# Performance work log

Measured on AMD Instinct MI355X. Metric: run time of the kernel, lower is better.

The kernel has to match this reference:

```python
import jax, jax.numpy as jnp
from jax import lax
import numpy as np

WIN = 11
PAD = WIN // 2
SIGMA = 1.5
GAMMA = 50.0


def _gauss_1d():
    x = jnp.arange(WIN, dtype=jnp.float32) - PAD
    g = jnp.exp(-(x * x) / (2.0 * SIGMA * SIGMA))
    return g / jnp.sum(g)


def _dwconv_gauss(x):
    # depthwise separable 11x11 gaussian blur, zero ('SAME') padding, NCHW
    C = x.shape[1]
    g = _gauss_1d()
    kh = jnp.tile(g.reshape(1, 1, WIN, 1), (C, 1, 1, 1))
    kw = jnp.tile(g.reshape(1, 1, 1, WIN), (C, 1, 1, 1))
    dn = ('NCHW', 'OIHW', 'NCHW')
    x = lax.conv_general_dilated(x, kh, (1, 1), [(PAD, PAD), (0, 0)],
                                 dimension_numbers=dn, feature_group_count=C)
    x = lax.conv_general_dilated(x, kw, (1, 1), [(0, 0), (PAD, PAD)],
                                 dimension_numbers=dn, feature_group_count=C)
    return x


def ssim(img1, img2):
    C1, C2 = 0.01 ** 2, 0.03 ** 2
    mu1 = _dwconv_gauss(img1)
    mu2 = _dwconv_gauss(img2)
    mu1_sq, mu2_sq, mu12 = mu1 * mu1, mu2 * mu2, mu1 * mu2
    sigma1_sq = _dwconv_gauss(img1 * img1) - mu1_sq
    sigma2_sq = _dwconv_gauss(img2 * img2) - mu2_sq
    sigma12 = _dwconv_gauss(img1 * img2) - mu12
    ssim_map = ((2 * mu12 + C1) * (2 * sigma12 + C2)) / (
        (mu1_sq + mu2_sq + C1) * (sigma1_sq + sigma2_sq + C2))
    return jnp.mean(ssim_map)


def warp(img, disp, x_dist, y_dist):
    # bilinear sample img at (x + x_dist*disp, y + y_dist*disp), border clamp
    B, C, H, W = img.shape
    d = disp[:, 0]  # [B,H,W]
    xs = jnp.arange(W, dtype=img.dtype)[None, None, :]
    ys = jnp.arange(H, dtype=img.dtype)[None, :, None]
    xn = jnp.clip(xs + x_dist * d, 0.0, W - 1.0)
    yn = jnp.clip(ys + y_dist * d, 0.0, H - 1.0)
    x0 = jnp.floor(xn)
    y0 = jnp.floor(yn)
    wx = xn - x0
    wy = yn - y0
    x0i = x0.astype(jnp.int32)
    y0i = y0.astype(jnp.int32)
    x1i = jnp.minimum(x0i + 1, W - 1)
    y1i = jnp.minimum(y0i + 1, H - 1)
    imh = jnp.transpose(img, (0, 2, 3, 1))  # [B,H,W,C]
    b = jnp.arange(B)[:, None, None]
    v00 = imh[b, y0i, x0i]
    v01 = imh[b, y0i, x1i]
    v10 = imh[b, y1i, x0i]
    v11 = imh[b, y1i, x1i]
    wx = wx[..., None]
    wy = wy[..., None]
    out = (v00 * (1 - wx) * (1 - wy) + v01 * wx * (1 - wy)
           + v10 * (1 - wx) * wy + v11 * wx * wy)
    return jnp.transpose(out, (0, 3, 1, 2))


def smooth_loss(disp, img, gamma):
    ddx = jnp.abs(disp[:, :, :, :-1] - disp[:, :, :, 1:])
    ddy = jnp.abs(disp[:, :, :-1, :] - disp[:, :, 1:, :])
    idx = jnp.mean(jnp.abs(img[:, :, :, :-1] - img[:, :, :, 1:]), axis=1, keepdims=True)
    idy = jnp.mean(jnp.abs(img[:, :, :-1, :] - img[:, :, 1:, :]), axis=1, keepdims=True)
    return jnp.mean(ddx * jnp.exp(-gamma * idx)) + jnp.mean(ddy * jnp.exp(-gamma * idy))


def l1(a, b):
    return jnp.mean(jnp.abs(a - b))


def setup_inputs() -> dict:
    key = jax.random.key(0)
    ks = jax.random.split(key, 8)
    B, H, W = 8, 512, 1024
    MAXD = 64.0
    return {
        'disp_l': jax.random.uniform(ks[0], (B, 1, H, W), jnp.float32) * MAXD,
        'disp_r': jax.random.uniform(ks[1], (B, 1, H, W), jnp.float32) * MAXD,
        'disp_ld2': jax.random.uniform(ks[2], (B, 1, H // 2, W // 2), jnp.float32) * (MAXD / 2),
        'disp_rd2': jax.random.uniform(ks[3], (B, 1, H // 2, W // 2), jnp.float32) * (MAXD / 2),
        'img_l': jax.random.uniform(ks[4], (B, 3, H, W), jnp.float32),
        'img_r': jax.random.uniform(ks[5], (B, 3, H, W), jnp.float32),
        'img_ld2': jax.random.uniform(ks[6], (B, 3, H // 2, W // 2), jnp.float32),
        'img_rd2': jax.random.uniform(ks[7], (B, 3, H // 2, W // 2), jnp.float32),
    }


def reference(disp_l, disp_r, disp_ld2, disp_rd2, img_l, img_r, img_ld2, img_rd2):
    img_ld2_warp = warp(img_rd2, disp_ld2, x_dist=-1.0, y_dist=0.0)
    img_rd2_warp = warp(img_ld2, disp_rd2, x_dist=1.0, y_dist=0.0)
    pm_d2 = l1(img_ld2_warp, img_ld2) + l1(img_rd2_warp, img_rd2)
    smooth_d2 = smooth_loss(disp_ld2, img_ld2, GAMMA) + smooth_loss(disp_rd2, img_rd2, GAMMA)

    img_l_warp = warp(img_r, disp_l, x_dist=-1.0, y_dist=0.0)
    img_r_warp = warp(img_l, disp_r, x_dist=1.0, y_dist=0.0)
    pm = l1(img_l_warp, img_l) + l1(img_r_warp, img_r)
    smooth = smooth_loss(disp_l, img_l, GAMMA) + smooth_loss(disp_r, img_r, GAMMA)
    ssim_loss = 1.0 - (ssim(img_l_warp, img_l) + ssim(img_r_warp, img_r)) / 2.0

    full_loss = pm_d2 + 0.1 * smooth_d2 + pm + ssim_loss + 0.1 * smooth
    monitor_loss = 5.0 * pm + ssim_loss
    return (full_loss, monitor_loss)
```

## Files before the change

kernel.cpp:

```cpp
#include <hip/hip_runtime.h>

#define B_ 8
#define C_ 3
#define H_ 512
#define W_ 1024
#define H2_ 256
#define W2_ 512
#define GAMMA_ 50.0f
#define NSUB 4

typedef __attribute__((ext_vector_type(2))) float v2f;


template <int NV>
__device__ __forceinline__ void reduce_acc(float (&v)[NV], double* acc, const int (&qidx)[NV]) {
    __shared__ float sred[NV][4];
    const int lane = threadIdx.x & 63;
    const int wave = threadIdx.x >> 6;
#pragma unroll
    for (int o = 32; o > 0; o >>= 1)
#pragma unroll
        for (int q = 0; q < NV; q++) v[q] += __shfl_down(v[q], o, 64);
    if (lane == 0)
#pragma unroll
        for (int q = 0; q < NV; q++) sred[q][wave] = v[q];
    __syncthreads();
    if (threadIdx.x == 0) {
        const int sub = blockIdx.x & (NSUB - 1);
#pragma unroll
        for (int q = 0; q < NV; q++) {
            float s = sred[q][0] + sred[q][1] + sred[q][2] + sred[q][3];
            atomicAdd(&acc[qidx[q] * NSUB + sub], (double)s);
        }
    }
}

__global__ void init_acc(double* acc) {
    if (threadIdx.x < 7 * NSUB) acc[threadIdx.x] = 0.0;
}

#define G0 0.0010283804f
#define G1 0.0075987582f
#define G2 0.0360007882f
#define G3 0.1093606949f
#define G4 0.2130055428f
#define G5 0.2660117248f

#define NHALF (B_ * H2_ * (W2_ / 4))
#define NSMOOTH (B_ * H_ * (W_ / 4))
#define NTOT (NHALF + NSMOOTH)

__global__ __launch_bounds__(256) void small_losses_kernel(
    const float* __restrict__ dL2, const float* __restrict__ dR2,
    const float* __restrict__ iL2, const float* __restrict__ iR2,
    const float* __restrict__ dL, const float* __restrict__ dR,
    const float* __restrict__ iL, const float* __restrict__ iR, double* acc) {
    float pm = 0.f, sx2 = 0.f, sy2 = 0.f, sxf = 0.f, syf = 0.f;
    for (int i = blockIdx.x * blockDim.x + threadIdx.x; i < NTOT;
         i += gridDim.x * blockDim.x) {
        if (i < NHALF) {
            const int W4 = W2_ >> 2;
            const int HW = H2_ * W2_;
            const int xq = i % W4;
            const int x4 = xq << 2;
            const int yz = i / W4;
            const int y = yz % H2_;
            const int b = yz / H2_;
            const int p0 = (b * H2_ + y) * W2_ + x4;
            const int ib = ((b * C_) * H2_ + y) * W2_ + x4;
            const bool lastx = (x4 + 4 == W2_);
            const bool lasty = (y == H2_ - 1);

            float dl[5], dr[5];
            *(float4*)dl = *(const float4*)(dL2 + p0);
            *(float4*)dr = *(const float4*)(dR2 + p0);
            dl[4] = lastx ? 0.f : dL2[p0 + 4];
            dr[4] = lastx ? 0.f : dR2[p0 + 4];

            int xl0[4], xl1[4], xr0[4], xr1[4];
            float wxl[4], wxr[4];
#pragma unroll
            for (int t = 0; t < 4; t++) {
                float xn = fminf(fmaxf((float)(x4 + t) - dl[t], 0.f), (float)(W2_ - 1));
                float xf = floorf(xn);
                wxl[t] = xn - xf;
                xl0[t] = (int)xf;
                xl1[t] = xl0[t] + (xl0[t] < W2_ - 1 ? 1 : 0);
                float xm = fminf(fmaxf((float)(x4 + t) + dr[t], 0.f), (float)(W2_ - 1));
                float xg = floorf(xm);
                wxr[t] = xm - xg;
                xr0[t] = (int)xg;
                xr1[t] = xr0[t] + (xr0[t] < W2_ - 1 ? 1 : 0);
            }

            float axL[4] = {0, 0, 0, 0}, axR[4] = {0, 0, 0, 0};
            float ayL[4] = {0, 0, 0, 0}, ayR[4] = {0, 0, 0, 0};
#pragma unroll
            for (int ch = 0; ch < C_; ch++) {
                const float* pL = iL2 + ib + ch * HW;
                const float* pR = iR2 + ib + ch * HW;
                float vL[5], vR[5];
                *(float4*)vL = *(const float4*)pL;
                *(float4*)vR = *(const float4*)pR;
                vL[4] = lastx ? 0.f : pL[4];
                vR[4] = lastx ? 0.f : pR[4];
#pragma unroll
                for (int t = 0; t < 4; t++) {
                    axL[t] += fabsf(vL[t] - vL[t + 1]);
                    axR[t] += fabsf(vR[t] - vR[t + 1]);
                }
                if (!lasty) {
                    float wLr[4], wRr[4];
                    *(float4*)wLr = *(const float4*)(pL + W2_);
                    *(float4*)wRr = *(const float4*)(pR + W2_);
#pragma unroll
                    for (int t = 0; t < 4; t++) {
                        ayL[t] += fabsf(vL[t] - wLr[t]);
                        ayR[t] += fabsf(vR[t] - wRr[t]);
                    }
                }
                const float* gLrow = iR2 + ib - x4 + ch * HW;
                const float* gRrow = iL2 + ib - x4 + ch * HW;
#pragma unroll
                for (int t = 0; t < 4; t++) {
                    float wv = gLrow[xl0[t]] * (1.f - wxl[t]) + gLrow[xl1[t]] * wxl[t];
                    pm += fabsf(wv - vL[t]);
                    float wv2 = gRrow[xr0[t]] * (1.f - wxr[t]) + gRrow[xr1[t]] * wxr[t];
                    pm += fabsf(wv2 - vR[t]);
                }
            }
            const int nx = lastx ? 3 : 4;
#pragma unroll
            for (int t = 0; t < 4; t++) {
                if (t < nx) {
                    sx2 += fabsf(dl[t] - dl[t + 1]) * __expf(-GAMMA_ * (axL[t] * (1.f / 3.f)));
                    sx2 += fabsf(dr[t] - dr[t + 1]) * __expf(-GAMMA_ * (axR[t] * (1.f / 3.f)));
                }
            }
            if (!lasty) {
                float el[4], er[4];
                *(float4*)el = *(const float4*)(dL2 + p0 + W2_);
                *(float4*)er = *(const float4*)(dR2 + p0 + W2_);
#pragma unroll
                for (int t = 0; t < 4; t++) {
                    sy2 += fabsf(dl[t] - el[t]) * __expf(-GAMMA_ * (ayL[t] * (1.f / 3.f)));
                    sy2 += fabsf(dr[t] - er[t]) * __expf(-GAMMA_ * (ayR[t] * (1.f / 3.f)));
                }
            }
        } else {
            const int s = i - NHALF;
            const int W4 = W_ >> 2;
            const int HW = H_ * W_;
            const int xq = s % W4;
            const int x4 = xq << 2;
            const int yz = s / W4;
            const int y = yz % H_;
            const int b = yz / H_;
            const int p0 = (b * H_ + y) * W_ + x4;
            const int ib = ((b * C_) * H_ + y) * W_ + x4;
            const bool lastx = (x4 + 4 == W_);
            const bool lasty = (y == H_ - 1);

            float axL[4] = {0, 0, 0, 0}, axR[4] = {0, 0, 0, 0};
            float ayL[4] = {0, 0, 0, 0}, ayR[4] = {0, 0, 0, 0};
#pragma unroll
            for (int ch = 0; ch < C_; ch++) {
                const float* pL = iL + ib + ch * HW;
                const float* pR = iR + ib + ch * HW;
                float vL[5], vR[5];
                *(float4*)vL = *(const float4*)pL;
                *(float4*)vR = *(const float4*)pR;
                vL[4] = lastx ? 0.f : pL[4];
                vR[4] = lastx ? 0.f : pR[4];
#pragma unroll
                for (int t = 0; t < 4; t++) {
                    axL[t] += fabsf(vL[t] - vL[t + 1]);
                    axR[t] += fabsf(vR[t] - vR[t + 1]);
                }
                if (!lasty) {
                    float wLr[4], wRr[4];
                    *(float4*)wLr = *(const float4*)(pL + W_);
                    *(float4*)wRr = *(const float4*)(pR + W_);
#pragma unroll
                    for (int t = 0; t < 4; t++) {
                        ayL[t] += fabsf(vL[t] - wLr[t]);
                        ayR[t] += fabsf(vR[t] - wRr[t]);
                    }
                }
            }
            float dl[5], dr[5];
            *(float4*)dl = *(const float4*)(dL + p0);
            *(float4*)dr = *(const float4*)(dR + p0);
            dl[4] = lastx ? 0.f : dL[p0 + 4];
            dr[4] = lastx ? 0.f : dR[p0 + 4];
            const int nx = lastx ? 3 : 4;
#pragma unroll
            for (int t = 0; t < 4; t++) {
                if (t < nx) {
                    sxf += fabsf(dl[t] - dl[t + 1]) * __expf(-GAMMA_ * (axL[t] * (1.f / 3.f)));
                    sxf += fabsf(dr[t] - dr[t + 1]) * __expf(-GAMMA_ * (axR[t] * (1.f / 3.f)));
                }
            }
            if (!lasty) {
                float el[4], er[4];
                *(float4*)el = *(const float4*)(dL + p0 + W_);
                *(float4*)er = *(const float4*)(dR + p0 + W_);
#pragma unroll
                for (int t = 0; t < 4; t++) {
                    syf += fabsf(dl[t] - el[t]) * __expf(-GAMMA_ * (ayL[t] * (1.f / 3.f)));
                    syf += fabsf(dr[t] - er[t]) * __expf(-GAMMA_ * (ayR[t] * (1.f / 3.f)));
                }
            }
        }
    }
    float vals[5] = {pm, sx2, sy2, sxf, syf};
    const int qidx[5] = {0, 1, 2, 4, 5};
    reduce_acc<5>(vals, acc, qidx);
}

#define TH 16
#define TW 64
#define HALO_H (TH + 10)
#define HALO_W (TW + 10)
#define HALO_N (HALO_H * HALO_W)
#define VW 75

__device__ __forceinline__ int swz(int ridx) {
    return ridx ^ (((ridx >> 3) & 1) << 1) ^ ((ridx >> 4) & 1);
}

__global__ __launch_bounds__(256) void ssim_pm_kernel(const float* __restrict__ img_l,
                                                      const float* __restrict__ img_r,
                                                      const float* __restrict__ disp_l,
                                                      const float* __restrict__ disp_r,
                                                      double* acc) {
    __shared__ float2 sAB[HALO_N];
    __shared__ float4 vF[TH * VW];

    const int z = blockIdx.z;
    const int b = z >> 1;
    const int pair = z & 1;
    const float* samp = (pair == 0) ? img_r : img_l;
    const float* targ = (pair == 0) ? img_l : img_r;
    const float* disp = (pair == 0) ? disp_l : disp_r;
    const float sign = (pair == 0) ? -1.f : 1.f;

    const int x0t = blockIdx.x * TW;
    const int y0t = blockIdx.y * TH;

    const float gg[11] = {G0, G1, G2, G3, G4, G5, G4, G3, G2, G1, G0};
    v2f w01[14], w23[14];
#pragma unroll
    for (int k = 0; k < 14; ++k) {
        w01[k].x = (k <= 10) ? gg[k] : 0.f;
        w01[k].y = (k >= 1 && k <= 11) ? gg[k - 1] : 0.f;
        w23[k].x = (k >= 2 && k <= 12) ? gg[k - 2] : 0.f;
        w23[k].y = (k >= 3) ? gg[k - 3] : 0.f;
    }

    int riy[8], gxa[8], gxb[8];
    float wxs[8];
    {
        const int bHW = b * (H_ * W_);
#pragma unroll
        for (int it = 0; it < 8; ++it) {
            const int idx = threadIdx.x + 256 * it;
            riy[it] = -1;
            if (idx < HALO_N) {
                const int i = idx / HALO_W;
                const int j = idx - i * HALO_W;
                const int iy = y0t + i - 5;
                const int ix = x0t + j - 5;
                if (iy >= 0 && iy < H_ && ix >= 0 && ix < W_) {
                    const int r = iy * W_ + ix;
                    riy[it] = r;
                    const float d = disp[bHW + r];
                    float xn = fminf(fmaxf((float)ix + sign * d, 0.f), (float)(W_ - 1));
                    float xf = floorf(xn);
                    wxs[it] = xn - xf;
                    const int xi = (int)xf;
                    gxa[it] = iy * W_ + xi;
                    gxb[it] = gxa[it] + (xi < W_ - 1 ? 1 : 0);
                }
            }
        }
    }

    float pa0[8], pa1[8], pbv[8];
    auto prefetch = [&](int c) {
        const int cb = (b * C_ + c) * (H_ * W_);
#pragma unroll
        for (int it = 0; it < 8; ++it) {
            const int idx = threadIdx.x + 256 * it;
            if (idx < HALO_N && riy[it] >= 0) {
                pbv[it] = targ[cb + riy[it]];
                pa0[it] = samp[cb + gxa[it]];
                pa1[it] = samp[cb + gxb[it]];
            }
        }
    };

    float ssim_loc = 0.f, pm_loc = 0.f;

    const int hr = threadIdx.x >> 4;
    const int hc0 = (threadIdx.x & 15) << 2;

    prefetch(0);

#pragma unroll 1
    for (int c = 0; c < C_; ++c) {
#pragma unroll
        for (int it = 0; it < 8; ++it) {
            const int idx = threadIdx.x + 256 * it;
            if (idx < HALO_N) {
                float av = 0.f, bv = 0.f;
                if (riy[it] >= 0) {
                    const float wx = wxs[it];
                    av = pa0[it] * (1.f - wx) + pa1[it] * wx;
                    bv = pbv[it];
                }
                sAB[idx] = make_float2(av, bv);
            }
        }
        __syncthreads();

        if (c + 1 < C_) prefetch(c + 1);

#pragma unroll
        for (int it = 0; it < 2; ++it) {
            const int t = threadIdx.x + 256 * it;
            if (t < 4 * HALO_W) {
                const int q = t / HALO_W;
                const int j = t - q * HALO_W;
                const int r0 = q * 4;
                const bool jc = (j >= 5 && j < 69);
                v2f amA = 0.f, bmA = 0.f, ssA = 0.f, abA = 0.f;
                v2f amB = 0.f, bmB = 0.f, ssB = 0.f, abB = 0.f;
#pragma unroll
                for (int k = 0; k < 14; ++k) {
                    const float2 p = sAB[(r0 + k) * HALO_W + j];
                    const float sq = fmaf(p.y, p.y, p.x * p.x);
                    const float ab = p.x * p.y;
                    const v2f wA = w01[k], wB = w23[k];
                    amA += wA * p.x;
                    bmA += wA * p.y;
                    ssA += wA * sq;
                    abA += wA * ab;
                    amB += wB * p.x;
                    bmB += wB * p.y;
                    ssB += wB * sq;
                    abB += wB * ab;
                    if (k >= 5 && k <= 8) {
                        if (jc) pm_loc += fabsf(p.x - p.y);
                    }
                }
                const int rb = r0 * VW + j;
                vF[swz(rb)] = make_float4(amA.x, bmA.x, ssA.x, abA.x);
                vF[swz(rb + VW)] = make_float4(amA.y, bmA.y, ssA.y, abA.y);
                vF[swz(rb + 2 * VW)] = make_float4(amB.x, bmB.x, ssB.x, abB.x);
                vF[swz(rb + 3 * VW)] = make_float4(amB.y, bmB.y, ssB.y, abB.y);
            }
        }
        __syncthreads();

        {
            const int rowb = hr * VW + hc0;
            v2f m1A = 0.f, m2A = 0.f, qsA = 0.f, q12A = 0.f;
            v2f m1B = 0.f, m2B = 0.f, qsB = 0.f, q12B = 0.f;
#pragma unroll
            for (int k = 0; k < 14; ++k) {
                const float4 f = vF[swz(rowb + k)];
                const v2f wA = w01[k], wB = w23[k];
                m1A += wA * f.x;
                m2A += wA * f.y;
                qsA += wA * f.z;
                q12A += wA * f.w;
                m1B += wB * f.x;
                m2B += wB * f.y;
                qsB += wB * f.z;
                q12B += wB * f.w;
            }
            const float C1 = 1e-4f, C2 = 9e-4f;
            {
                const v2f mu1sq = m1A * m1A, mu2sq = m2A * m2A, mu12 = m1A * m2A;
                const v2f s12 = q12A - mu12, ss = qsA - mu1sq - mu2sq;
                const v2f num = (2.f * mu12 + C1) * (2.f * s12 + C2);
                const v2f den = (mu1sq + mu2sq + C1) * (ss + C2);
                const v2f r = num / den;
                ssim_loc += r.x + r.y;
            }
            {
                const v2f mu1sq = m1B * m1B, mu2sq = m2B * m2B, mu12 = m1B * m2B;
                const v2f s12 = q12B - mu12, ss = qsB - mu1sq - mu2sq;
                const v2f num = (2.f * mu12 + C1) * (2.f * s12 + C2);
                const v2f den = (mu1sq + mu2sq + C1) * (ss + C2);
                const v2f r = num / den;
                ssim_loc += r.x + r.y;
            }
        }
    }

    float vals[2] = {ssim_loc, pm_loc};
    const int qidx[2] = {6, 3};
    reduce_acc<2>(vals, acc, qidx);
}

__global__ void finalize_kernel(const double* __restrict__ acc, float* __restrict__ out) {
    if (threadIdx.x == 0 && blockIdx.x == 0) {
        double q[7];
        for (int i = 0; i < 7; i++) {
            q[i] = 0.0;
            for (int s = 0; s < NSUB; s++) q[i] += acc[i * NSUB + s];
        }
        const double N2 = (double)B_ * C_ * H2_ * W2_;
        const double Nx2 = (double)B_ * H2_ * (W2_ - 1);
        const double Ny2 = (double)B_ * (H2_ - 1) * W2_;
        const double N1 = (double)B_ * C_ * H_ * W_;
        const double Nx1 = (double)B_ * H_ * (W_ - 1);
        const double Ny1 = (double)B_ * (H_ - 1) * W_;
        double pm_d2 = q[0] / N2;
        double smooth_d2 = q[1] / Nx2 + q[2] / Ny2;
        double pm = q[3] / N1;
        double smooth = q[4] / Nx1 + q[5] / Ny1;
        double ssim_loss = 1.0 - q[6] / (2.0 * N1);
        double full = pm_d2 + 0.1 * smooth_d2 + pm + ssim_loss + 0.1 * smooth;
        double mon = 5.0 * pm + ssim_loss;
        out[0] = (float)full;
        out[1] = (float)mon;
    }
}

extern "C" void kernel_launch(void* const* d_in, const int* in_sizes, int n_in,
                              void* d_out, int out_size, void* d_ws, size_t ws_size,
                              hipStream_t stream) {
    const float* disp_l = (const float*)d_in[0];
    const float* disp_r = (const float*)d_in[1];
    const float* disp_ld2 = (const float*)d_in[2];
    const float* disp_rd2 = (const float*)d_in[3];
    const float* img_l = (const float*)d_in[4];
    const float* img_r = (const float*)d_in[5];
    const float* img_ld2 = (const float*)d_in[6];
    const float* img_rd2 = (const float*)d_in[7];
    double* acc = (double*)d_ws;
    float* out = (float*)d_out;

    hipLaunchKernelGGL(init_acc, dim3(1), dim3(64), 0, stream, acc);

    hipLaunchKernelGGL(small_losses_kernel, dim3(2048), dim3(256), 0, stream,
                       disp_ld2, disp_rd2, img_ld2, img_rd2,
                       disp_l, disp_r, img_l, img_r, acc);

    dim3 grid(W_ / TW, H_ / TH, 2 * B_);
    hipLaunchKernelGGL(ssim_pm_kernel, grid, dim3(256), 0, stream,
                       img_l, img_r, disp_l, disp_r, acc);

    hipLaunchKernelGGL(finalize_kernel, dim3(1), dim3(1), 0, stream, acc, out);
}
```

Baseline: 231.1 us.

## Fuse small-loss and SSIM kernels into one interleaved-grid launch

```diff
diff --git a/kernel.cpp b/kernel.cpp
--- a/kernel.cpp
+++ b/kernel.cpp
@@ -46,178 +46,6 @@
 #define G4 0.2130055428f
 #define G5 0.2660117248f
 
-#define NHALF (B_ * H2_ * (W2_ / 4))
-#define NSMOOTH (B_ * H_ * (W_ / 4))
-#define NTOT (NHALF + NSMOOTH)
-
-__global__ __launch_bounds__(256) void small_losses_kernel(
-    const float* __restrict__ dL2, const float* __restrict__ dR2,
-    const float* __restrict__ iL2, const float* __restrict__ iR2,
-    const float* __restrict__ dL, const float* __restrict__ dR,
-    const float* __restrict__ iL, const float* __restrict__ iR, double* acc) {
-    float pm = 0.f, sx2 = 0.f, sy2 = 0.f, sxf = 0.f, syf = 0.f;
-    for (int i = blockIdx.x * blockDim.x + threadIdx.x; i < NTOT;
-         i += gridDim.x * blockDim.x) {
-        if (i < NHALF) {
-            const int W4 = W2_ >> 2;
-            const int HW = H2_ * W2_;
-            const int xq = i % W4;
-            const int x4 = xq << 2;
-            const int yz = i / W4;
-            const int y = yz % H2_;
-            const int b = yz / H2_;
-            const int p0 = (b * H2_ + y) * W2_ + x4;
-            const int ib = ((b * C_) * H2_ + y) * W2_ + x4;
-            const bool lastx = (x4 + 4 == W2_);
-            const bool lasty = (y == H2_ - 1);
-
-            float dl[5], dr[5];
-            *(float4*)dl = *(const float4*)(dL2 + p0);
-            *(float4*)dr = *(const float4*)(dR2 + p0);
-            dl[4] = lastx ? 0.f : dL2[p0 + 4];
-            dr[4] = lastx ? 0.f : dR2[p0 + 4];
-
-            int xl0[4], xl1[4], xr0[4], xr1[4];
-            float wxl[4], wxr[4];
-#pragma unroll
-            for (int t = 0; t < 4; t++) {
-                float xn = fminf(fmaxf((float)(x4 + t) - dl[t], 0.f), (float)(W2_ - 1));
-                float xf = floorf(xn);
-                wxl[t] = xn - xf;
-                xl0[t] = (int)xf;
-                xl1[t] = xl0[t] + (xl0[t] < W2_ - 1 ? 1 : 0);
-                float xm = fminf(fmaxf((float)(x4 + t) + dr[t], 0.f), (float)(W2_ - 1));
-                float xg = floorf(xm);
-                wxr[t] = xm - xg;
-                xr0[t] = (int)xg;
-                xr1[t] = xr0[t] + (xr0[t] < W2_ - 1 ? 1 : 0);
-            }
-
-            float axL[4] = {0, 0, 0, 0}, axR[4] = {0, 0, 0, 0};
-            float ayL[4] = {0, 0, 0, 0}, ayR[4] = {0, 0, 0, 0};
-#pragma unroll
-            for (int ch = 0; ch < C_; ch++) {
-                const float* pL = iL2 + ib + ch * HW;
-                const float* pR = iR2 + ib + ch * HW;
-                float vL[5], vR[5];
-                *(float4*)vL = *(const float4*)pL;
-                *(float4*)vR = *(const float4*)pR;
-                vL[4] = lastx ? 0.f : pL[4];
-                vR[4] = lastx ? 0.f : pR[4];
-#pragma unroll
-                for (int t = 0; t < 4; t++) {
-                    axL[t] += fabsf(vL[t] - vL[t + 1]);
-                    axR[t] += fabsf(vR[t] - vR[t + 1]);
-                }
-                if (!lasty) {
-                    float wLr[4], wRr[4];
-                    *(float4*)wLr = *(const float4*)(pL + W2_);
-                    *(float4*)wRr = *(const float4*)(pR + W2_);
-#pragma unroll
-                    for (int t = 0; t < 4; t++) {
-                        ayL[t] += fabsf(vL[t] - wLr[t]);
-                        ayR[t] += fabsf(vR[t] - wRr[t]);
-                    }
-                }
-                const float* gLrow = iR2 + ib - x4 + ch * HW;
-                const float* gRrow = iL2 + ib - x4 + ch * HW;
-#pragma unroll
-                for (int t = 0; t < 4; t++) {
-                    float wv = gLrow[xl0[t]] * (1.f - wxl[t]) + gLrow[xl1[t]] * wxl[t];
-                    pm += fabsf(wv - vL[t]);
-                    float wv2 = gRrow[xr0[t]] * (1.f - wxr[t]) + gRrow[xr1[t]] * wxr[t];
-                    pm += fabsf(wv2 - vR[t]);
-                }
-            }
-            const int nx = lastx ? 3 : 4;
-#pragma unroll
-            for (int t = 0; t < 4; t++) {
-                if (t < nx) {
-                    sx2 += fabsf(dl[t] - dl[t + 1]) * __expf(-GAMMA_ * (axL[t] * (1.f / 3.f)));
-                    sx2 += fabsf(dr[t] - dr[t + 1]) * __expf(-GAMMA_ * (axR[t] * (1.f / 3.f)));
-                }
-            }
-            if (!lasty) {
-                float el[4], er[4];
-                *(float4*)el = *(const float4*)(dL2 + p0 + W2_);
-                *(float4*)er = *(const float4*)(dR2 + p0 + W2_);
-#pragma unroll
-                for (int t = 0; t < 4; t++) {
-                    sy2 += fabsf(dl[t] - el[t]) * __expf(-GAMMA_ * (ayL[t] * (1.f / 3.f)));
-                    sy2 += fabsf(dr[t] - er[t]) * __expf(-GAMMA_ * (ayR[t] * (1.f / 3.f)));
-                }
-            }
-        } else {
-            const int s = i - NHALF;
-            const int W4 = W_ >> 2;
-            const int HW = H_ * W_;
-            const int xq = s % W4;
-            const int x4 = xq << 2;
-            const int yz = s / W4;
-            const int y = yz % H_;
-            const int b = yz / H_;
-            const int p0 = (b * H_ + y) * W_ + x4;
-            const int ib = ((b * C_) * H_ + y) * W_ + x4;
-            const bool lastx = (x4 + 4 == W_);
-            const bool lasty = (y == H_ - 1);
-
-            float axL[4] = {0, 0, 0, 0}, axR[4] = {0, 0, 0, 0};
-            float ayL[4] = {0, 0, 0, 0}, ayR[4] = {0, 0, 0, 0};
-#pragma unroll
-            for (int ch = 0; ch < C_; ch++) {
-                const float* pL = iL + ib + ch * HW;
-                const float* pR = iR + ib + ch * HW;
-                float vL[5], vR[5];
-                *(float4*)vL = *(const float4*)pL;
-                *(float4*)vR = *(const float4*)pR;
-                vL[4] = lastx ? 0.f : pL[4];
-                vR[4] = lastx ? 0.f : pR[4];
-#pragma unroll
-                for (int t = 0; t < 4; t++) {
-                    axL[t] += fabsf(vL[t] - vL[t + 1]);
-                    axR[t] += fabsf(vR[t] - vR[t + 1]);
-                }
-                if (!lasty) {
-                    float wLr[4], wRr[4];
-                    *(float4*)wLr = *(const float4*)(pL + W_);
-                    *(float4*)wRr = *(const float4*)(pR + W_);
-#pragma unroll
-                    for (int t = 0; t < 4; t++) {
-                        ayL[t] += fabsf(vL[t] - wLr[t]);
-                        ayR[t] += fabsf(vR[t] - wRr[t]);
-                    }
-                }
-            }
-            float dl[5], dr[5];
-            *(float4*)dl = *(const float4*)(dL + p0);
-            *(float4*)dr = *(const float4*)(dR + p0);
-            dl[4] = lastx ? 0.f : dL[p0 + 4];
-            dr[4] = lastx ? 0.f : dR[p0 + 4];
-            const int nx = lastx ? 3 : 4;
-#pragma unroll
-            for (int t = 0; t < 4; t++) {
-                if (t < nx) {
-                    sxf += fabsf(dl[t] - dl[t + 1]) * __expf(-GAMMA_ * (axL[t] * (1.f / 3.f)));
-                    sxf += fabsf(dr[t] - dr[t + 1]) * __expf(-GAMMA_ * (axR[t] * (1.f / 3.f)));
-                }
-            }
-            if (!lasty) {
-                float el[4], er[4];
-                *(float4*)el = *(const float4*)(dL + p0 + W_);
-                *(float4*)er = *(const float4*)(dR + p0 + W_);
-#pragma unroll
-                for (int t = 0; t < 4; t++) {
-                    syf += fabsf(dl[t] - el[t]) * __expf(-GAMMA_ * (ayL[t] * (1.f / 3.f)));
-                    syf += fabsf(dr[t] - er[t]) * __expf(-GAMMA_ * (ayR[t] * (1.f / 3.f)));
-                }
-            }
-        }
-    }
-    float vals[5] = {pm, sx2, sy2, sxf, syf};
-    const int qidx[5] = {0, 1, 2, 4, 5};
-    reduce_acc<5>(vals, acc, qidx);
-}
-
 #define TH 16
 #define TW 64
 #define HALO_H (TH + 10)
@@ -225,19 +53,197 @@
 #define HALO_N (HALO_H * HALO_W)
 #define VW 75
 
+#define NHALF (B_ * H2_ * (W2_ / 4))
+#define NSMOOTH (B_ * H_ * (W_ / 4))
+#define NTOT (NHALF + NSMOOTH)
+#define NSMALLBLK 1024
+#define NSSIMBLK 8192
+
 __device__ __forceinline__ int swz(int ridx) {
     return ridx ^ (((ridx >> 3) & 1) << 1) ^ ((ridx >> 4) & 1);
 }
 
-__global__ __launch_bounds__(256) void ssim_pm_kernel(const float* __restrict__ img_l,
-                                                      const float* __restrict__ img_r,
-                                                      const float* __restrict__ disp_l,
-                                                      const float* __restrict__ disp_r,
-                                                      double* acc) {
+__global__ __launch_bounds__(256) void fused_kernel(
+    const float* __restrict__ disp_l, const float* __restrict__ disp_r,
+    const float* __restrict__ dL2, const float* __restrict__ dR2,
+    const float* __restrict__ img_l, const float* __restrict__ img_r,
+    const float* __restrict__ iL2, const float* __restrict__ iR2, double* acc) {
     __shared__ float2 sAB[HALO_N];
     __shared__ float4 vF[TH * VW];
 
-    const int z = blockIdx.z;
+    const int bid = blockIdx.x;
+    const int grp = bid / 9;
+    const int rem = bid - grp * 9;
+
+    if (rem == 8) {
+        float pm = 0.f, sx2 = 0.f, sy2 = 0.f, sxf = 0.f, syf = 0.f;
+        for (int i = grp * blockDim.x + threadIdx.x; i < NTOT;
+             i += NSMALLBLK * blockDim.x) {
+            if (i < NHALF) {
+                const int W4 = W2_ >> 2;
+                const int HW = H2_ * W2_;
+                const int xq = i % W4;
+                const int x4 = xq << 2;
+                const int yz = i / W4;
+                const int y = yz % H2_;
+                const int b = yz / H2_;
+                const int p0 = (b * H2_ + y) * W2_ + x4;
+                const int ib = ((b * C_) * H2_ + y) * W2_ + x4;
+                const bool lastx = (x4 + 4 == W2_);
+                const bool lasty = (y == H2_ - 1);
+
+                float dl[5], dr[5];
+                *(float4*)dl = *(const float4*)(dL2 + p0);
+                *(float4*)dr = *(const float4*)(dR2 + p0);
+                dl[4] = lastx ? 0.f : dL2[p0 + 4];
+                dr[4] = lastx ? 0.f : dR2[p0 + 4];
+
+                int xl0[4], xl1[4], xr0[4], xr1[4];
+                float wxl[4], wxr[4];
+#pragma unroll
+                for (int t = 0; t < 4; t++) {
+                    float xn = fminf(fmaxf((float)(x4 + t) - dl[t], 0.f), (float)(W2_ - 1));
+                    float xf = floorf(xn);
+                    wxl[t] = xn - xf;
+                    xl0[t] = (int)xf;
+                    xl1[t] = xl0[t] + (xl0[t] < W2_ - 1 ? 1 : 0);
+                    float xm = fminf(fmaxf((float)(x4 + t) + dr[t], 0.f), (float)(W2_ - 1));
+                    float xg = floorf(xm);
+                    wxr[t] = xm - xg;
+                    xr0[t] = (int)xg;
+                    xr1[t] = xr0[t] + (xr0[t] < W2_ - 1 ? 1 : 0);
+                }
+
+                float axL[4] = {0, 0, 0, 0}, axR[4] = {0, 0, 0, 0};
+                float ayL[4] = {0, 0, 0, 0}, ayR[4] = {0, 0, 0, 0};
+#pragma unroll
+                for (int ch = 0; ch < C_; ch++) {
+                    const float* pL = iL2 + ib + ch * HW;
+                    const float* pR = iR2 + ib + ch * HW;
+                    float vL[5], vR[5];
+                    *(float4*)vL = *(const float4*)pL;
+                    *(float4*)vR = *(const float4*)pR;
+                    vL[4] = lastx ? 0.f : pL[4];
+                    vR[4] = lastx ? 0.f : pR[4];
+#pragma unroll
+                    for (int t = 0; t < 4; t++) {
+                        axL[t] += fabsf(vL[t] - vL[t + 1]);
+                        axR[t] += fabsf(vR[t] - vR[t + 1]);
+                    }
+                    if (!lasty) {
+                        float wLr[4], wRr[4];
+                        *(float4*)wLr = *(const float4*)(pL + W2_);
+                        *(float4*)wRr = *(const float4*)(pR + W2_);
+#pragma unroll
+                        for (int t = 0; t < 4; t++) {
+                            ayL[t] += fabsf(vL[t] - wLr[t]);
+                            ayR[t] += fabsf(vR[t] - wRr[t]);
+                        }
+                    }
+                    const float* gLrow = iR2 + ib - x4 + ch * HW;
+                    const float* gRrow = iL2 + ib - x4 + ch * HW;
+#pragma unroll
+                    for (int t = 0; t < 4; t++) {
+                        float wv = gLrow[xl0[t]] * (1.f - wxl[t]) + gLrow[xl1[t]] * wxl[t];
+                        pm += fabsf(wv - vL[t]);
+                        float wv2 = gRrow[xr0[t]] * (1.f - wxr[t]) + gRrow[xr1[t]] * wxr[t];
+                        pm += fabsf(wv2 - vR[t]);
+                    }
+                }
+                const int nx = lastx ? 3 : 4;
+#pragma unroll
+                for (int t = 0; t < 4; t++) {
+                    if (t < nx) {
+                        sx2 += fabsf(dl[t] - dl[t + 1]) * __expf(-GAMMA_ * (axL[t] * (1.f / 3.f)));
+                        sx2 += fabsf(dr[t] - dr[t + 1]) * __expf(-GAMMA_ * (axR[t] * (1.f / 3.f)));
+                    }
+                }
+                if (!lasty) {
+                    float el[4], er[4];
+                    *(float4*)el = *(const float4*)(dL2 + p0 + W2_);
+                    *(float4*)er = *(const float4*)(dR2 + p0 + W2_);
+#pragma unroll
+                    for (int t = 0; t < 4; t++) {
+                        sy2 += fabsf(dl[t] - el[t]) * __expf(-GAMMA_ * (ayL[t] * (1.f / 3.f)));
+                        sy2 += fabsf(dr[t] - er[t]) * __expf(-GAMMA_ * (ayR[t] * (1.f / 3.f)));
+                    }
+                }
+            } else {
+                const int s = i - NHALF;
+                const int W4 = W_ >> 2;
+                const int HW = H_ * W_;
+                const int xq = s % W4;
+                const int x4 = xq << 2;
+                const int yz = s / W4;
+                const int y = yz % H_;
+                const int b = yz / H_;
+                const int p0 = (b * H_ + y) * W_ + x4;
+                const int ib = ((b * C_) * H_ + y) * W_ + x4;
+                const bool lastx = (x4 + 4 == W_);
+                const bool lasty = (y == H_ - 1);
+
+                float axL[4] = {0, 0, 0, 0}, axR[4] = {0, 0, 0, 0};
+                float ayL[4] = {0, 0, 0, 0}, ayR[4] = {0, 0, 0, 0};
+#pragma unroll
+                for (int ch = 0; ch < C_; ch++) {
+                    const float* pL = img_l + ib + ch * HW;
+                    const float* pR = img_r + ib + ch * HW;
+                    float vL[5], vR[5];
+                    *(float4*)vL = *(const float4*)pL;
+                    *(float4*)vR = *(const float4*)pR;
+                    vL[4] = lastx ? 0.f : pL[4];
+                    vR[4] = lastx ? 0.f : pR[4];
+#pragma unroll
+                    for (int t = 0; t < 4; t++) {
+                        axL[t] += fabsf(vL[t] - vL[t + 1]);
+                        axR[t] += fabsf(vR[t] - vR[t + 1]);
+                    }
+                    if (!lasty) {
+                        float wLr[4], wRr[4];
+                        *(float4*)wLr = *(const float4*)(pL + W_);
+                        *(float4*)wRr = *(const float4*)(pR + W_);
+#pragma unroll
+                        for (int t = 0; t < 4; t++) {
+                            ayL[t] += fabsf(vL[t] - wLr[t]);
+                            ayR[t] += fabsf(vR[t] - wRr[t]);
+                        }
+                    }
+                }
+                float dl[5], dr[5];
+                *(float4*)dl = *(const float4*)(disp_l + p0);
+                *(float4*)dr = *(const float4*)(disp_r + p0);
+                dl[4] = lastx ? 0.f : disp_l[p0 + 4];
+                dr[4] = lastx ? 0.f : disp_r[p0 + 4];
+                const int nx = lastx ? 3 : 4;
+#pragma unroll
+                for (int t = 0; t < 4; t++) {
+                    if (t < nx) {
+                        sxf += fabsf(dl[t] - dl[t + 1]) * __expf(-GAMMA_ * (axL[t] * (1.f / 3.f)));
+                        sxf += fabsf(dr[t] - dr[t + 1]) * __expf(-GAMMA_ * (axR[t] * (1.f / 3.f)));
+                    }
+                }
+                if (!lasty) {
+                    float el[4], er[4];
+                    *(float4*)el = *(const float4*)(disp_l + p0 + W_);
+                    *(float4*)er = *(const float4*)(disp_r + p0 + W_);
+#pragma unroll
+                    for (int t = 0; t < 4; t++) {
+                        syf += fabsf(dl[t] - el[t]) * __expf(-GAMMA_ * (ayL[t] * (1.f / 3.f)));
+                        syf += fabsf(dr[t] - er[t]) * __expf(-GAMMA_ * (ayR[t] * (1.f / 3.f)));
+                    }
+                }
+            }
+        }
+        float vals[5] = {pm, sx2, sy2, sxf, syf};
+        const int qidx[5] = {0, 1, 2, 4, 5};
+        reduce_acc<5>(vals, acc, qidx);
+        return;
+    }
+
+    const int sid = grp * 8 + rem;
+    const int bx = sid & 15;
+    const int by = (sid >> 4) & 31;
+    const int z = sid >> 9;
     const int b = z >> 1;
     const int pair = z & 1;
     const float* samp = (pair == 0) ? img_r : img_l;
@@ -245,8 +251,8 @@
     const float* disp = (pair == 0) ? disp_l : disp_r;
     const float sign = (pair == 0) ? -1.f : 1.f;
 
-    const int x0t = blockIdx.x * TW;
-    const int y0t = blockIdx.y * TH;
+    const int x0t = bx * TW;
+    const int y0t = by * TH;
 
     const float gg[11] = {G0, G1, G2, G3, G4, G5, G4, G3, G2, G1, G0};
     v2f w01[14], w23[14];
@@ -446,13 +452,9 @@
 
     hipLaunchKernelGGL(init_acc, dim3(1), dim3(64), 0, stream, acc);
 
-    hipLaunchKernelGGL(small_losses_kernel, dim3(2048), dim3(256), 0, stream,
-                       disp_ld2, disp_rd2, img_ld2, img_rd2,
-                       disp_l, disp_r, img_l, img_r, acc);
-
-    dim3 grid(W_ / TW, H_ / TH, 2 * B_);
-    hipLaunchKernelGGL(ssim_pm_kernel, grid, dim3(256), 0, stream,
-                       img_l, img_r, disp_l, disp_r, acc);
+    hipLaunchKernelGGL(fused_kernel, dim3(NSSIMBLK + NSMALLBLK), dim3(256), 0, stream,
+                       disp_l, disp_r, disp_ld2, disp_rd2,
+                       img_l, img_r, img_ld2, img_rd2, acc);
 
     hipLaunchKernelGGL(finalize_kernel, dim3(1), dim3(1), 0, stream, acc, out);
 }
```

After: 196.1 us. 15.1% less time.
